# Performance work log

Measured on AMD Instinct MI355X. Metric: run time of the kernel, lower is better.

Reference implementation:

```python
import jax, jax.numpy as jnp
import numpy as np

SIGMA = 5.0  # matches init_kwargs sigma


def so3_exp_map(w):
    """Rodrigues formula. w: [..., 3] axis-angle -> [..., 3, 3] rotation."""
    theta = jnp.sqrt(jnp.sum(w * w, axis=-1) + 1e-12)            # [...]
    wx, wy, wz = w[..., 0], w[..., 1], w[..., 2]
    z = jnp.zeros_like(wx)
    # normalized skew matrix K = hat(w) / theta
    K = jnp.stack([z, -wz, wy,
                   wz, z, -wx,
                   -wy, wx, z], axis=-1).reshape(w.shape[:-1] + (3, 3))
    K = K / theta[..., None, None]
    s = jnp.sin(theta)[..., None, None]
    c = (1.0 - jnp.cos(theta))[..., None, None]
    I = jnp.eye(3, dtype=w.dtype)
    return I + s * K + c * (K @ K)


def setup_inputs() -> dict:
    key = jax.random.key(0)
    k1, k2, k3, k4, k5 = jax.random.split(key, 5)
    P, N, E = 65536, 512, 4096
    # spread points/control points over a volume where sigma=5 is a meaningful scale
    points = jax.random.normal(k1, (P, 3), dtype=jnp.float32) * 10.0
    control_points = jax.random.normal(k2, (N, 3), dtype=jnp.float32) * 10.0
    rot_vec = jax.random.normal(k3, (N, 3), dtype=jnp.float32) * 0.1
    t = jax.random.normal(k4, (N, 3), dtype=jnp.float32) * 0.1
    edges = jax.random.randint(k5, (E, 2), 0, N, dtype=jnp.int64)
    return {"points": points, "control_points": control_points,
            "rot_vec": rot_vec, "t": t, "edges": edges}


def reference(points, control_points, rot_vec, t, edges):
    # ---- warp_points ----
    # local: [P, N, 3]
    local = points[:, None, :] - control_points[None, :, :]
    skin = jnp.exp(-jnp.sum(local * local, axis=-1) / (2.0 * SIGMA * SIGMA))  # [P, N]
    skin = skin / (jnp.sum(skin, axis=-1, keepdims=True) + 1e-5)
    R = so3_exp_map(rot_vec)                                    # [N, 3, 3]
    warped = (jnp.einsum('nij,pnj->pni', R, local)
              + t[None, :, :] + control_points[None, :, :])     # [P, N, 3]
    warped = jnp.sum(warped * skin[..., None], axis=1)          # [P, 3]
    # ---- reg_term ----
    i, j = edges[:, 0], edges[:, 1]
    ci, cj = control_points[i], control_points[j]               # [E, 3]
    ti, tj = t[i], t[j]
    Ri = R[i]                                                   # [E, 3, 3]
    resid = jnp.einsum('mij,mj->mi', Ri, cj - ci) + ci + ti - (cj + tj)
    reg = jnp.sum(resid * resid)
    return warped, reg
```

## Files before the change

kernel.cpp:

```cpp
#include <hip/hip_runtime.h>
#include <math.h>


constexpr int NP = 65536;
constexpr int NN = 512;
constexpr int NE = 4096;
constexpr int PPB = 256;
constexpr int CH = 4;
constexpr int NPC = NN / CH;
constexpr float KEXP = -0.02f * 1.44269504088896340736f;
constexpr float M2K = -2.0f * KEXP;

#if defined(__has_builtin)
#if __has_builtin(__builtin_amdgcn_exp2f)
#define FAST_EXP2(x) __builtin_amdgcn_exp2f(x)
#endif
#endif
#ifndef FAST_EXP2
#define FAST_EXP2(x) exp2f(x)
#endif

__device__ __forceinline__ void rodrigues(float wx, float wy, float wz, float* R) {
    float t2 = wx * wx + wy * wy + wz * wz + 1e-12f;
    float th = sqrtf(t2);
    float inv = 1.0f / th;
    float kx = wx * inv, ky = wy * inv, kz = wz * inv;
    float s = sinf(th);
    float c = 1.0f - cosf(th);
    float kxky = kx * ky, kxkz = kx * kz, kykz = ky * kz;
    R[0] = 1.0f - c * (ky * ky + kz * kz);
    R[1] = -s * kz + c * kxky;
    R[2] =  s * ky + c * kxkz;
    R[3] =  s * kz + c * kxky;
    R[4] = 1.0f - c * (kx * kx + kz * kz);
    R[5] = -s * kx + c * kykz;
    R[6] = -s * ky + c * kxkz;
    R[7] =  s * kx + c * kykz;
    R[8] = 1.0f - c * (kx * kx + ky * ky);
}

__global__ __launch_bounds__(1024) void deform_kernel(
    const float* __restrict__ points,
    const float* __restrict__ cps,
    const float* __restrict__ rot,
    const float* __restrict__ tr,
    const int* __restrict__ edges,
    float* __restrict__ out)
{
    __shared__ float nd[NN * 16];
    __shared__ float4 red[CH - 1][PPB];
    __shared__ float red2[16];

    const int bid = blockIdx.x;
    const int tid = threadIdx.x;

    if (bid < NP / PPB) {
        for (int n = tid; n < NN; n += 1024) {
            float R[9];
            rodrigues(rot[3 * n + 0], rot[3 * n + 1], rot[3 * n + 2], R);
            float cx = cps[3 * n + 0], cy = cps[3 * n + 1], cz = cps[3 * n + 2];
            float tx = tr[3 * n + 0], ty = tr[3 * n + 1], tz = tr[3 * n + 2];
            float bx = tx + cx - (R[0] * cx + R[1] * cy + R[2] * cz);
            float by = ty + cy - (R[3] * cx + R[4] * cy + R[5] * cz);
            float bz = tz + cz - (R[6] * cx + R[7] * cy + R[8] * cz);
            float kc2 = KEXP * (cx * cx + cy * cy + cz * cz);
            float* r = &nd[n * 16];
            r[0] = R[0]; r[1] = R[1]; r[2] = R[2]; r[3] = R[3];
            r[4] = R[4]; r[5] = R[5]; r[6] = R[6]; r[7] = R[7];
            r[8] = R[8]; r[9] = bx;  r[10] = by;  r[11] = bz;
            r[12] = cx;  r[13] = cy; r[14] = cz;  r[15] = kc2;
        }
        __syncthreads();

        const int pt = tid & (PPB - 1);
        const int chunk = tid >> 8;
        const int p = bid * PPB + pt;
        const float px = points[3 * p + 0];
        const float py = points[3 * p + 1];
        const float pz = points[3 * p + 2];
        const float kp2 = KEXP * (px * px + py * py + pz * pz);

        float ax = 0.0f, ay = 0.0f, az = 0.0f, wsum = 0.0f;
        const float* base = &nd[chunk * NPC * 16];

        #pragma unroll 4
        for (int n = 0; n < NPC; ++n) {
            const float4* q = (const float4*)(base + n * 16);
            float4 q0 = q[0];
            float4 q1 = q[1];
            float4 q2 = q[2];
            float4 q3 = q[3];
            float dot = fmaf(q3.x, px, fmaf(q3.y, py, q3.z * pz));
            float w = FAST_EXP2(fmaf(M2K, dot, kp2 + q3.w));
            float yx = fmaf(q0.x, px, fmaf(q0.y, py, fmaf(q0.z, pz, q2.y)));
            float yy = fmaf(q0.w, px, fmaf(q1.x, py, fmaf(q1.y, pz, q2.z)));
            float yz = fmaf(q1.z, px, fmaf(q1.w, py, fmaf(q2.x, pz, q2.w)));
            wsum += w;
            ax = fmaf(w, yx, ax);
            ay = fmaf(w, yy, ay);
            az = fmaf(w, yz, az);
        }

        if (chunk != 0) {
            red[chunk - 1][pt] = make_float4(ax, ay, az, wsum);
        }
        __syncthreads();
        if (chunk == 0) {
            #pragma unroll
            for (int r = 0; r < CH - 1; ++r) {
                float4 v = red[r][pt];
                ax += v.x; ay += v.y; az += v.z; wsum += v.w;
            }
            float invw = 1.0f / (wsum + 1e-5f);
            out[3 * p + 0] = ax * invw;
            out[3 * p + 1] = ay * invw;
            out[3 * p + 2] = az * invw;
        }
    } else {
        float acc = 0.0f;
        for (int e = tid; e < NE; e += 1024) {
            int i = edges[2 * e + 0];
            int j = edges[2 * e + 1];
            float R[9];
            rodrigues(rot[3 * i + 0], rot[3 * i + 1], rot[3 * i + 2], R);
            float cix = cps[3 * i + 0], ciy = cps[3 * i + 1], ciz = cps[3 * i + 2];
            float cjx = cps[3 * j + 0], cjy = cps[3 * j + 1], cjz = cps[3 * j + 2];
            float dx = cjx - cix, dy = cjy - ciy, dz = cjz - ciz;
            float rx = fmaf(R[0], dx, fmaf(R[1], dy, R[2] * dz)) + cix + tr[3 * i + 0] - cjx - tr[3 * j + 0];
            float ry = fmaf(R[3], dx, fmaf(R[4], dy, R[5] * dz)) + ciy + tr[3 * i + 1] - cjy - tr[3 * j + 1];
            float rz = fmaf(R[6], dx, fmaf(R[7], dy, R[8] * dz)) + ciz + tr[3 * i + 2] - cjz - tr[3 * j + 2];
            acc += rx * rx + ry * ry + rz * rz;
        }
        #pragma unroll
        for (int off = 32; off > 0; off >>= 1)
            acc += __shfl_down(acc, off, 64);
        int wid = tid >> 6;
        if ((tid & 63) == 0) red2[wid] = acc;
        __syncthreads();
        if (tid == 0) {
            float s = 0.0f;
            #pragma unroll
            for (int i = 0; i < 16; ++i) s += red2[i];
            out[3 * NP] = s;
        }
    }
}

extern "C" void kernel_launch(void* const* d_in, const int* in_sizes, int n_in,
                              void* d_out, int out_size, void* d_ws, size_t ws_size,
                              hipStream_t stream) {
    const float* points = (const float*)d_in[0];
    const float* cps    = (const float*)d_in[1];
    const float* rot    = (const float*)d_in[2];
    const float* tr     = (const float*)d_in[3];
    const int*   edges  = (const int*)d_in[4];
    float* out = (float*)d_out;
    deform_kernel<<<NP / PPB + 1, 1024, 0, stream>>>(points, cps, rot, tr, edges, out);
}
```

Measured before the change: 89.34 us.

## Register-block four points per thread and split control points into sixteen chunks

Each thread now handles four points, so every control-point record read from LDS is reused across four points instead of one. Control points are split into sixteen chunks per 64-thread wavefront group, and partial sums are combined with a tree reduction through shared memory. Points are loaded and outputs stored as float4 vectors. The cost targeted is LDS bandwidth per FLOP. In exchange it adds register pressure, more reduction barriers, and a larger shared reduction buffer.

```diff
diff --git a/kernel.cpp b/kernel.cpp
--- a/kernel.cpp
+++ b/kernel.cpp
@@ -5,8 +5,10 @@
 constexpr int NP = 65536;
 constexpr int NN = 512;
 constexpr int NE = 4096;
-constexpr int PPB = 256;
-constexpr int CH = 4;
+constexpr int PPT = 4;
+constexpr int CH = 16;
+constexpr int TPC = 64;
+constexpr int PPB = TPC * PPT;
 constexpr int NPC = NN / CH;
 constexpr float KEXP = -0.02f * 1.44269504088896340736f;
 constexpr float M2K = -2.0f * KEXP;
@@ -48,14 +50,15 @@
     float* __restrict__ out)
 {
     __shared__ float nd[NN * 16];
-    __shared__ float4 red[CH - 1][PPB];
+    __shared__ float4 red[CH / 2][PPB];
     __shared__ float red2[16];
 
     const int bid = blockIdx.x;
     const int tid = threadIdx.x;
 
     if (bid < NP / PPB) {
-        for (int n = tid; n < NN; n += 1024) {
+        if (tid < NN) {
+            int n = tid;
             float R[9];
             rodrigues(rot[3 * n + 0], rot[3 * n + 1], rot[3 * n + 2], R);
             float cx = cps[3 * n + 0], cy = cps[3 * n + 1], cz = cps[3 * n + 2];
@@ -72,49 +75,75 @@
         }
         __syncthreads();
 
-        const int pt = tid & (PPB - 1);
-        const int chunk = tid >> 8;
-        const int p = bid * PPB + pt;
-        const float px = points[3 * p + 0];
-        const float py = points[3 * p + 1];
-        const float pz = points[3 * p + 2];
-        const float kp2 = KEXP * (px * px + py * py + pz * pz);
+        const int chunk = tid >> 6;
+        const int tslot = tid & 63;
+        const int p0 = bid * PPB + tslot * PPT;
 
-        float ax = 0.0f, ay = 0.0f, az = 0.0f, wsum = 0.0f;
+        const float4* pv = (const float4*)(points + 3 * p0);
+        float4 va = pv[0], vb = pv[1], vc = pv[2];
+        float px[PPT] = {va.x, va.w, vb.z, vc.y};
+        float py[PPT] = {va.y, vb.x, vb.w, vc.z};
+        float pz[PPT] = {va.z, vb.y, vc.x, vc.w};
+        float kp2[PPT];
+        #pragma unroll
+        for (int k = 0; k < PPT; ++k)
+            kp2[k] = KEXP * (px[k] * px[k] + py[k] * py[k] + pz[k] * pz[k]);
+
+        float ax[PPT] = {0,0,0,0}, ay[PPT] = {0,0,0,0}, az[PPT] = {0,0,0,0}, ws[PPT] = {0,0,0,0};
         const float* base = &nd[chunk * NPC * 16];
 
-        #pragma unroll 4
+        #pragma unroll 2
         for (int n = 0; n < NPC; ++n) {
             const float4* q = (const float4*)(base + n * 16);
             float4 q0 = q[0];
             float4 q1 = q[1];
             float4 q2 = q[2];
             float4 q3 = q[3];
-            float dot = fmaf(q3.x, px, fmaf(q3.y, py, q3.z * pz));
-            float w = FAST_EXP2(fmaf(M2K, dot, kp2 + q3.w));
-            float yx = fmaf(q0.x, px, fmaf(q0.y, py, fmaf(q0.z, pz, q2.y)));
-            float yy = fmaf(q0.w, px, fmaf(q1.x, py, fmaf(q1.y, pz, q2.z)));
-            float yz = fmaf(q1.z, px, fmaf(q1.w, py, fmaf(q2.x, pz, q2.w)));
-            wsum += w;
-            ax = fmaf(w, yx, ax);
-            ay = fmaf(w, yy, ay);
-            az = fmaf(w, yz, az);
+            #pragma unroll
+            for (int k = 0; k < PPT; ++k) {
+                float dot = fmaf(q3.x, px[k], fmaf(q3.y, py[k], q3.z * pz[k]));
+                float w = FAST_EXP2(fmaf(M2K, dot, kp2[k] + q3.w));
+                float yx = fmaf(q0.x, px[k], fmaf(q0.y, py[k], fmaf(q0.z, pz[k], q2.y)));
+                float yy = fmaf(q0.w, px[k], fmaf(q1.x, py[k], fmaf(q1.y, pz[k], q2.z)));
+                float yz = fmaf(q1.z, px[k], fmaf(q1.w, py[k], fmaf(q2.x, pz[k], q2.w)));
+                ws[k] += w;
+                ax[k] = fmaf(w, yx, ax[k]);
+                ay[k] = fmaf(w, yy, ay[k]);
+                az[k] = fmaf(w, yz, az[k]);
+            }
         }
 
-        if (chunk != 0) {
-            red[chunk - 1][pt] = make_float4(ax, ay, az, wsum);
+        #pragma unroll
+        for (int s = CH / 2; s >= 1; s >>= 1) {
+            if (chunk >= s && chunk < 2 * s) {
+                #pragma unroll
+                for (int k = 0; k < PPT; ++k)
+                    red[chunk - s][tslot * PPT + k] = make_float4(ax[k], ay[k], az[k], ws[k]);
+            }
+            __syncthreads();
+            if (chunk < s) {
+                #pragma unroll
+                for (int k = 0; k < PPT; ++k) {
+                    float4 v = red[chunk][tslot * PPT + k];
+                    ax[k] += v.x; ay[k] += v.y; az[k] += v.z; ws[k] += v.w;
+                }
+            }
+            __syncthreads();
         }
-        __syncthreads();
+
         if (chunk == 0) {
+            float o[12];
             #pragma unroll
-            for (int r = 0; r < CH - 1; ++r) {
-                float4 v = red[r][pt];
-                ax += v.x; ay += v.y; az += v.z; wsum += v.w;
+            for (int k = 0; k < PPT; ++k) {
+                float invw = 1.0f / (ws[k] + 1e-5f);
+                o[3 * k + 0] = ax[k] * invw;
+                o[3 * k + 1] = ay[k] * invw;
+                o[3 * k + 2] = az[k] * invw;
             }
-            float invw = 1.0f / (wsum + 1e-5f);
-            out[3 * p + 0] = ax * invw;
-            out[3 * p + 1] = ay * invw;
-            out[3 * p + 2] = az * invw;
+            float4* ov = (float4*)(out + 3 * p0);
+            ov[0] = make_float4(o[0], o[1], o[2], o[3]);
+            ov[1] = make_float4(o[4], o[5], o[6], o[7]);
+            ov[2] = make_float4(o[8], o[9], o[10], o[11]);
         }
     } else {
         float acc = 0.0f;
```

Result: faster. 85.94 us (-3.8%).

## Split prep into separate kernel and stream node table via scalar loads

Applied to the files above, without the earlier changes.

Moves per-node Rodrigues and bias precomputation into a small prep kernel that writes a 16-float table to workspace, instead of recomputing it into shared memory in every block. The main warp kernel then reads each node record with inline-asm s_load_dwordx16 into scalar registers, so the LDS reads and the per-block prep and barrier go away. Blocks now handle 128 points with 8 node chunks per point. Each table read waits immediately on lgkmcnt(0), which serialises scalar-load latency. The extra kernel launch adds a dependency between the two kernels.

```diff
diff --git a/kernel.cpp b/kernel.cpp
--- a/kernel.cpp
+++ b/kernel.cpp
@@ -5,11 +5,13 @@
 constexpr int NP = 65536;
 constexpr int NN = 512;
 constexpr int NE = 4096;
-constexpr int PPB = 256;
-constexpr int CH = 4;
+constexpr int CH = 8;
+constexpr int TPC = 128;
 constexpr int NPC = NN / CH;
 constexpr float KEXP = -0.02f * 1.44269504088896340736f;
 constexpr float M2K = -2.0f * KEXP;
+
+typedef float f16v __attribute__((ext_vector_type(16)));
 
 #if defined(__has_builtin)
 #if __has_builtin(__builtin_amdgcn_exp2f)
@@ -39,23 +41,13 @@
     R[8] = 1.0f - c * (kx * kx + ky * ky);
 }
 
-__global__ __launch_bounds__(1024) void deform_kernel(
-    const float* __restrict__ points,
-    const float* __restrict__ cps,
-    const float* __restrict__ rot,
-    const float* __restrict__ tr,
-    const int* __restrict__ edges,
-    float* __restrict__ out)
-{
-    __shared__ float nd[NN * 16];
-    __shared__ float4 red[CH - 1][PPB];
-    __shared__ float red2[16];
-
-    const int bid = blockIdx.x;
+__global__ void prep_kernel(const float* __restrict__ cps, const float* __restrict__ rot,
+                            const float* __restrict__ tr, const int* __restrict__ edges,
+                            float* __restrict__ tbl, float* __restrict__ out) {
     const int tid = threadIdx.x;
-
-    if (bid < NP / PPB) {
-        for (int n = tid; n < NN; n += 1024) {
+    if (blockIdx.x == 0) {
+        if (tid < NN) {
+            const int n = tid;
             float R[9];
             rodrigues(rot[3 * n + 0], rot[3 * n + 1], rot[3 * n + 2], R);
             float cx = cps[3 * n + 0], cy = cps[3 * n + 1], cz = cps[3 * n + 2];
@@ -64,61 +56,15 @@
             float by = ty + cy - (R[3] * cx + R[4] * cy + R[5] * cz);
             float bz = tz + cz - (R[6] * cx + R[7] * cy + R[8] * cz);
             float kc2 = KEXP * (cx * cx + cy * cy + cz * cz);
-            float* r = &nd[n * 16];
-            r[0] = R[0]; r[1] = R[1]; r[2] = R[2]; r[3] = R[3];
-            r[4] = R[4]; r[5] = R[5]; r[6] = R[6]; r[7] = R[7];
-            r[8] = R[8]; r[9] = bx;  r[10] = by;  r[11] = bz;
-            r[12] = cx;  r[13] = cy; r[14] = cz;  r[15] = kc2;
-        }
-        __syncthreads();
-
-        const int pt = tid & (PPB - 1);
-        const int chunk = tid >> 8;
-        const int p = bid * PPB + pt;
-        const float px = points[3 * p + 0];
-        const float py = points[3 * p + 1];
-        const float pz = points[3 * p + 2];
-        const float kp2 = KEXP * (px * px + py * py + pz * pz);
-
-        float ax = 0.0f, ay = 0.0f, az = 0.0f, wsum = 0.0f;
-        const float* base = &nd[chunk * NPC * 16];
-
-        #pragma unroll 4
-        for (int n = 0; n < NPC; ++n) {
-            const float4* q = (const float4*)(base + n * 16);
-            float4 q0 = q[0];
-            float4 q1 = q[1];
-            float4 q2 = q[2];
-            float4 q3 = q[3];
-            float dot = fmaf(q3.x, px, fmaf(q3.y, py, q3.z * pz));
-            float w = FAST_EXP2(fmaf(M2K, dot, kp2 + q3.w));
-            float yx = fmaf(q0.x, px, fmaf(q0.y, py, fmaf(q0.z, pz, q2.y)));
-            float yy = fmaf(q0.w, px, fmaf(q1.x, py, fmaf(q1.y, pz, q2.z)));
-            float yz = fmaf(q1.z, px, fmaf(q1.w, py, fmaf(q2.x, pz, q2.w)));
-            wsum += w;
-            ax = fmaf(w, yx, ax);
-            ay = fmaf(w, yy, ay);
-            az = fmaf(w, yz, az);
-        }
-
-        if (chunk != 0) {
-            red[chunk - 1][pt] = make_float4(ax, ay, az, wsum);
-        }
-        __syncthreads();
-        if (chunk == 0) {
-            #pragma unroll
-            for (int r = 0; r < CH - 1; ++r) {
-                float4 v = red[r][pt];
-                ax += v.x; ay += v.y; az += v.z; wsum += v.w;
-            }
-            float invw = 1.0f / (wsum + 1e-5f);
-            out[3 * p + 0] = ax * invw;
-            out[3 * p + 1] = ay * invw;
-            out[3 * p + 2] = az * invw;
+            float4* r = (float4*)(tbl + n * 16);
+            r[0] = make_float4(R[0], R[1], R[2], R[3]);
+            r[1] = make_float4(R[4], R[5], R[6], R[7]);
+            r[2] = make_float4(R[8], bx, by, bz);
+            r[3] = make_float4(cx, cy, cz, kc2);
         }
     } else {
         float acc = 0.0f;
-        for (int e = tid; e < NE; e += 1024) {
+        for (int e = tid; e < NE; e += 512) {
             int i = edges[2 * e + 0];
             int j = edges[2 * e + 1];
             float R[9];
@@ -131,6 +77,7 @@
             float rz = fmaf(R[6], dx, fmaf(R[7], dy, R[8] * dz)) + ciz + tr[3 * i + 2] - cjz - tr[3 * j + 2];
             acc += rx * rx + ry * ry + rz * rz;
         }
+        __shared__ float red2[8];
         #pragma unroll
         for (int off = 32; off > 0; off >>= 1)
             acc += __shfl_down(acc, off, 64);
@@ -140,9 +87,62 @@
         if (tid == 0) {
             float s = 0.0f;
             #pragma unroll
-            for (int i = 0; i < 16; ++i) s += red2[i];
+            for (int i = 0; i < 8; ++i) s += red2[i];
             out[3 * NP] = s;
         }
+    }
+}
+
+__global__ __launch_bounds__(1024, 8) void warp_kernel(
+    const float* __restrict__ points,
+    const float* __restrict__ tbl,
+    float* __restrict__ out)
+{
+    __shared__ float4 red[CH - 1][TPC];
+
+    const int tid = threadIdx.x;
+    const int pt = tid & (TPC - 1);
+    const int chunk = tid >> 7;
+    const int p = blockIdx.x * TPC + pt;
+
+    const float px = points[3 * p + 0];
+    const float py = points[3 * p + 1];
+    const float pz = points[3 * p + 2];
+    const float kp2 = KEXP * (px * px + py * py + pz * pz);
+
+    float ax = 0.0f, ay = 0.0f, az = 0.0f, ws = 0.0f;
+
+    const float* ap = tbl + (size_t)(unsigned)__builtin_amdgcn_readfirstlane(chunk * (NPC * 16));
+
+    for (int n = 0; n < NPC; ++n) {
+        f16v r;
+        asm("s_load_dwordx16 %0, %1, 0x0\n\ts_waitcnt lgkmcnt(0)"
+            : "=s"(r) : "s"(ap));
+        ap += 16;
+        float dot = fmaf(r[12], px, fmaf(r[13], py, r[14] * pz));
+        float arg = fmaf(M2K, dot, kp2 + r[15]);
+        float w = FAST_EXP2(arg);
+        float yx = fmaf(r[0], px, fmaf(r[1], py, fmaf(r[2], pz, r[9])));
+        float yy = fmaf(r[3], px, fmaf(r[4], py, fmaf(r[5], pz, r[10])));
+        float yz = fmaf(r[6], px, fmaf(r[7], py, fmaf(r[8], pz, r[11])));
+        ws += w;
+        ax = fmaf(w, yx, ax);
+        ay = fmaf(w, yy, ay);
+        az = fmaf(w, yz, az);
+    }
+
+    if (chunk != 0) red[chunk - 1][pt] = make_float4(ax, ay, az, ws);
+    __syncthreads();
+    if (chunk == 0) {
+        #pragma unroll
+        for (int s = 0; s < CH - 1; ++s) {
+            float4 v = red[s][pt];
+            ax += v.x; ay += v.y; az += v.z; ws += v.w;
+        }
+        float invw = 1.0f / (ws + 1e-5f);
+        out[3 * p + 0] = ax * invw;
+        out[3 * p + 1] = ay * invw;
+        out[3 * p + 2] = az * invw;
     }
 }
 
@@ -155,5 +155,8 @@
     const float* tr     = (const float*)d_in[3];
     const int*   edges  = (const int*)d_in[4];
     float* out = (float*)d_out;
-    deform_kernel<<<NP / PPB + 1, 1024, 0, stream>>>(points, cps, rot, tr, edges, out);
+    float* tbl = (float*)d_ws;
+
+    prep_kernel<<<2, 512, 0, stream>>>(cps, rot, tr, edges, tbl, out);
+    warp_kernel<<<NP / TPC, 1024, 0, stream>>>(points, tbl, out);
 }
```

Measured after the change: 92.39 us. 1.03x slower.

## Register-tile eight points per thread with packed FP32 math and fused reg term

Applied to the files above, without the earlier changes.

Each thread now processes 8 points as packed float2 vectors, so every control-point record loaded from LDS is reused across 8 points, and the math can map to packed FMA instructions. The 512 control points are split across 32 chunks. Partial sums are reduced with a cross-half-wave shuffle and then a tree reduction through LDS. The separate regularisation block is removed: each block handles 16 edges using the precomputed shared table and atomically adds into the scalar output. Risks: the atomicAdd relies on the output already being zero, higher register pressure, and extra synchronisation in the tree reduction.

```diff
diff --git a/kernel.cpp b/kernel.cpp
--- a/kernel.cpp
+++ b/kernel.cpp
@@ -6,10 +6,13 @@
 constexpr int NN = 512;
 constexpr int NE = 4096;
 constexpr int PPB = 256;
-constexpr int CH = 4;
+constexpr int PPT = 8;
+constexpr int CH = 32;
 constexpr int NPC = NN / CH;
 constexpr float KEXP = -0.02f * 1.44269504088896340736f;
 constexpr float M2K = -2.0f * KEXP;
+
+typedef float f2 __attribute__((ext_vector_type(2)));
 
 #if defined(__has_builtin)
 #if __has_builtin(__builtin_amdgcn_exp2f)
@@ -19,6 +22,14 @@
 #ifndef FAST_EXP2
 #define FAST_EXP2(x) exp2f(x)
 #endif
+
+__device__ __forceinline__ f2 b2(float s) { f2 r; r.x = s; r.y = s; return r; }
+__device__ __forceinline__ f2 fm(f2 a, f2 b, f2 c) { return __builtin_elementwise_fma(a, b, c); }
+__device__ __forceinline__ f2 xadd32(f2 v) {
+    v.x += __shfl_xor(v.x, 32, 64);
+    v.y += __shfl_xor(v.y, 32, 64);
+    return v;
+}
 
 __device__ __forceinline__ void rodrigues(float wx, float wy, float wz, float* R) {
     float t2 = wx * wx + wy * wy + wz * wz + 1e-12f;
@@ -39,7 +50,7 @@
     R[8] = 1.0f - c * (kx * kx + ky * ky);
 }
 
-__global__ __launch_bounds__(1024) void deform_kernel(
+__global__ __launch_bounds__(1024, 4) void deform_kernel(
     const float* __restrict__ points,
     const float* __restrict__ cps,
     const float* __restrict__ rot,
@@ -48,101 +59,135 @@
     float* __restrict__ out)
 {
     __shared__ float nd[NN * 16];
-    __shared__ float4 red[CH - 1][PPB];
-    __shared__ float red2[16];
+    __shared__ float4 stab[NN];
+    __shared__ float4 slab[8][PPB];
 
     const int bid = blockIdx.x;
     const int tid = threadIdx.x;
 
-    if (bid < NP / PPB) {
-        for (int n = tid; n < NN; n += 1024) {
-            float R[9];
-            rodrigues(rot[3 * n + 0], rot[3 * n + 1], rot[3 * n + 2], R);
-            float cx = cps[3 * n + 0], cy = cps[3 * n + 1], cz = cps[3 * n + 2];
-            float tx = tr[3 * n + 0], ty = tr[3 * n + 1], tz = tr[3 * n + 2];
-            float bx = tx + cx - (R[0] * cx + R[1] * cy + R[2] * cz);
-            float by = ty + cy - (R[3] * cx + R[4] * cy + R[5] * cz);
-            float bz = tz + cz - (R[6] * cx + R[7] * cy + R[8] * cz);
-            float kc2 = KEXP * (cx * cx + cy * cy + cz * cz);
-            float* r = &nd[n * 16];
-            r[0] = R[0]; r[1] = R[1]; r[2] = R[2]; r[3] = R[3];
-            r[4] = R[4]; r[5] = R[5]; r[6] = R[6]; r[7] = R[7];
-            r[8] = R[8]; r[9] = bx;  r[10] = by;  r[11] = bz;
-            r[12] = cx;  r[13] = cy; r[14] = cz;  r[15] = kc2;
+    if (tid < NN) {
+        const int n = tid;
+        float R[9];
+        rodrigues(rot[3 * n + 0], rot[3 * n + 1], rot[3 * n + 2], R);
+        float cx = cps[3 * n + 0], cy = cps[3 * n + 1], cz = cps[3 * n + 2];
+        float tx = tr[3 * n + 0], ty = tr[3 * n + 1], tz = tr[3 * n + 2];
+        float bx = tx + cx - (R[0] * cx + R[1] * cy + R[2] * cz);
+        float by = ty + cy - (R[3] * cx + R[4] * cy + R[5] * cz);
+        float bz = tz + cz - (R[6] * cx + R[7] * cy + R[8] * cz);
+        float kc2 = KEXP * (cx * cx + cy * cy + cz * cz);
+        float4* r = (float4*)(&nd[n * 16]);
+        r[0] = make_float4(R[0], R[1], R[2], R[3]);
+        r[1] = make_float4(R[4], R[5], R[6], R[7]);
+        r[2] = make_float4(R[8], bx, by, bz);
+        r[3] = make_float4(cx, cy, cz, kc2);
+        stab[n] = make_float4(cx + tx, cy + ty, cz + tz, 0.0f);
+    }
+    __syncthreads();
+
+    if (tid < 16) {
+        const int e = bid * 16 + tid;
+        const int i = edges[2 * e + 0];
+        const int j = edges[2 * e + 1];
+        const float4* ri = (const float4*)(&nd[i * 16]);
+        float4 q0 = ri[0], q1 = ri[1], q2 = ri[2];
+        float4 cj = ((const float4*)(&nd[j * 16]))[3];
+        float4 sj = stab[j];
+        float rx = fmaf(q0.x, cj.x, fmaf(q0.y, cj.y, fmaf(q0.z, cj.z, q2.y))) - sj.x;
+        float ry = fmaf(q0.w, cj.x, fmaf(q1.x, cj.y, fmaf(q1.y, cj.z, q2.z))) - sj.y;
+        float rz = fmaf(q1.z, cj.x, fmaf(q1.w, cj.y, fmaf(q2.x, cj.z, q2.w))) - sj.z;
+        float acc = rx * rx + ry * ry + rz * rz;
+        #pragma unroll
+        for (int off = 8; off > 0; off >>= 1)
+            acc += __shfl_down(acc, off, 16);
+        if (tid == 0) atomicAdd(out + 3 * NP, acc);
+    }
+
+    const int pslot = tid & 31;
+    const int chunk = tid >> 5;
+    const int p0 = bid * PPB + pslot * PPT;
+
+    const float4* pv = (const float4*)(points + 3 * p0);
+    float4 A = pv[0], B = pv[1], Cv = pv[2], D = pv[3], E = pv[4], F = pv[5];
+    f2 px[4], py[4], pz[4];
+    px[0].x=A.x;  px[0].y=A.w;  py[0].x=A.y;  py[0].y=B.x;  pz[0].x=A.z;  pz[0].y=B.y;
+    px[1].x=B.z;  px[1].y=Cv.y; py[1].x=B.w;  py[1].y=Cv.z; pz[1].x=Cv.x; pz[1].y=Cv.w;
+    px[2].x=D.x;  px[2].y=D.w;  py[2].x=D.y;  py[2].y=E.x;  pz[2].x=D.z;  pz[2].y=E.y;
+    px[3].x=E.z;  px[3].y=F.y;  py[3].x=E.w;  py[3].y=F.z;  pz[3].x=F.x;  pz[3].y=F.w;
+
+    f2 kp2[4], ax[4], ay[4], az[4], ws[4];
+    #pragma unroll
+    for (int k = 0; k < 4; ++k) {
+        kp2[k] = b2(KEXP) * (px[k] * px[k] + py[k] * py[k] + pz[k] * pz[k]);
+        ax[k] = b2(0.0f); ay[k] = b2(0.0f); az[k] = b2(0.0f); ws[k] = b2(0.0f);
+    }
+
+    const float* base = &nd[chunk * NPC * 16];
+    #pragma unroll 2
+    for (int n = 0; n < NPC; ++n) {
+        const float4* q = (const float4*)(base + n * 16);
+        float4 q0 = q[0], q1 = q[1], q2 = q[2], q3 = q[3];
+        #pragma unroll
+        for (int k = 0; k < 4; ++k) {
+            f2 dot = fm(b2(q3.x), px[k], fm(b2(q3.y), py[k], b2(q3.z) * pz[k]));
+            f2 arg = fm(b2(M2K), dot, kp2[k] + b2(q3.w));
+            f2 w; w.x = FAST_EXP2(arg.x); w.y = FAST_EXP2(arg.y);
+            f2 yx = fm(b2(q0.x), px[k], fm(b2(q0.y), py[k], fm(b2(q0.z), pz[k], b2(q2.y))));
+            f2 yy = fm(b2(q0.w), px[k], fm(b2(q1.x), py[k], fm(b2(q1.y), pz[k], b2(q2.z))));
+            f2 yz = fm(b2(q1.z), px[k], fm(b2(q1.w), py[k], fm(b2(q2.x), pz[k], b2(q2.w))));
+            ws[k] += w;
+            ax[k] = fm(w, yx, ax[k]);
+            ay[k] = fm(w, yy, ay[k]);
+            az[k] = fm(w, yz, az[k]);
+        }
+    }
+
+    #pragma unroll
+    for (int k = 0; k < 4; ++k) {
+        ax[k] = xadd32(ax[k]); ay[k] = xadd32(ay[k]);
+        az[k] = xadd32(az[k]); ws[k] = xadd32(ws[k]);
+    }
+
+    const int wv = tid >> 6;
+    const bool lo = (tid & 32) == 0;
+    #pragma unroll
+    for (int s = 8; s >= 1; s >>= 1) {
+        if (lo && wv >= s && wv < 2 * s) {
+            #pragma unroll
+            for (int k = 0; k < 4; ++k) {
+                int i0 = pslot * 8 + ((2 * k + pslot) & 7);
+                int i1 = pslot * 8 + ((2 * k + 1 + pslot) & 7);
+                slab[wv - s][i0] = make_float4(ax[k].x, ay[k].x, az[k].x, ws[k].x);
+                slab[wv - s][i1] = make_float4(ax[k].y, ay[k].y, az[k].y, ws[k].y);
+            }
         }
         __syncthreads();
-
-        const int pt = tid & (PPB - 1);
-        const int chunk = tid >> 8;
-        const int p = bid * PPB + pt;
-        const float px = points[3 * p + 0];
-        const float py = points[3 * p + 1];
-        const float pz = points[3 * p + 2];
-        const float kp2 = KEXP * (px * px + py * py + pz * pz);
-
-        float ax = 0.0f, ay = 0.0f, az = 0.0f, wsum = 0.0f;
-        const float* base = &nd[chunk * NPC * 16];
-
-        #pragma unroll 4
-        for (int n = 0; n < NPC; ++n) {
-            const float4* q = (const float4*)(base + n * 16);
-            float4 q0 = q[0];
-            float4 q1 = q[1];
-            float4 q2 = q[2];
-            float4 q3 = q[3];
-            float dot = fmaf(q3.x, px, fmaf(q3.y, py, q3.z * pz));
-            float w = FAST_EXP2(fmaf(M2K, dot, kp2 + q3.w));
-            float yx = fmaf(q0.x, px, fmaf(q0.y, py, fmaf(q0.z, pz, q2.y)));
-            float yy = fmaf(q0.w, px, fmaf(q1.x, py, fmaf(q1.y, pz, q2.z)));
-            float yz = fmaf(q1.z, px, fmaf(q1.w, py, fmaf(q2.x, pz, q2.w)));
-            wsum += w;
-            ax = fmaf(w, yx, ax);
-            ay = fmaf(w, yy, ay);
-            az = fmaf(w, yz, az);
-        }
-
-        if (chunk != 0) {
-            red[chunk - 1][pt] = make_float4(ax, ay, az, wsum);
+        if (lo && wv < s) {
+            #pragma unroll
+            for (int k = 0; k < 4; ++k) {
+                int i0 = pslot * 8 + ((2 * k + pslot) & 7);
+                int i1 = pslot * 8 + ((2 * k + 1 + pslot) & 7);
+                float4 v0 = slab[wv][i0];
+                float4 v1 = slab[wv][i1];
+                ax[k].x += v0.x; ay[k].x += v0.y; az[k].x += v0.z; ws[k].x += v0.w;
+                ax[k].y += v1.x; ay[k].y += v1.y; az[k].y += v1.z; ws[k].y += v1.w;
+            }
         }
         __syncthreads();
-        if (chunk == 0) {
-            #pragma unroll
-            for (int r = 0; r < CH - 1; ++r) {
-                float4 v = red[r][pt];
-                ax += v.x; ay += v.y; az += v.z; wsum += v.w;
-            }
-            float invw = 1.0f / (wsum + 1e-5f);
-            out[3 * p + 0] = ax * invw;
-            out[3 * p + 1] = ay * invw;
-            out[3 * p + 2] = az * invw;
-        }
-    } else {
-        float acc = 0.0f;
-        for (int e = tid; e < NE; e += 1024) {
-            int i = edges[2 * e + 0];
-            int j = edges[2 * e + 1];
-            float R[9];
-            rodrigues(rot[3 * i + 0], rot[3 * i + 1], rot[3 * i + 2], R);
-            float cix = cps[3 * i + 0], ciy = cps[3 * i + 1], ciz = cps[3 * i + 2];
-            float cjx = cps[3 * j + 0], cjy = cps[3 * j + 1], cjz = cps[3 * j + 2];
-            float dx = cjx - cix, dy = cjy - ciy, dz = cjz - ciz;
-            float rx = fmaf(R[0], dx, fmaf(R[1], dy, R[2] * dz)) + cix + tr[3 * i + 0] - cjx - tr[3 * j + 0];
-            float ry = fmaf(R[3], dx, fmaf(R[4], dy, R[5] * dz)) + ciy + tr[3 * i + 1] - cjy - tr[3 * j + 1];
-            float rz = fmaf(R[6], dx, fmaf(R[7], dy, R[8] * dz)) + ciz + tr[3 * i + 2] - cjz - tr[3 * j + 2];
-            acc += rx * rx + ry * ry + rz * rz;
-        }
-        #pragma unroll
-        for (int off = 32; off > 0; off >>= 1)
-            acc += __shfl_down(acc, off, 64);
-        int wid = tid >> 6;
-        if ((tid & 63) == 0) red2[wid] = acc;
-        __syncthreads();
-        if (tid == 0) {
-            float s = 0.0f;
-            #pragma unroll
-            for (int i = 0; i < 16; ++i) s += red2[i];
-            out[3 * NP] = s;
-        }
+    }
+
+    if (tid < 32) {
+        float o[24];
+        #pragma unroll
+        for (int k = 0; k < 4; ++k) {
+            float ivx = 1.0f / (ws[k].x + 1e-5f);
+            float ivy = 1.0f / (ws[k].y + 1e-5f);
+            o[6 * k + 0] = ax[k].x * ivx; o[6 * k + 1] = ay[k].x * ivx; o[6 * k + 2] = az[k].x * ivx;
+            o[6 * k + 3] = ax[k].y * ivy; o[6 * k + 4] = ay[k].y * ivy; o[6 * k + 5] = az[k].y * ivy;
+        }
+        float4* ov = (float4*)(out + 3 * p0);
+        #pragma unroll
+        for (int q = 0; q < 6; ++q)
+            ov[q] = make_float4(o[4 * q], o[4 * q + 1], o[4 * q + 2], o[4 * q + 3]);
     }
 }
 
@@ -155,5 +200,5 @@
     const float* tr     = (const float*)d_in[3];
     const int*   edges  = (const int*)d_in[4];
     float* out = (float*)d_out;
-    deform_kernel<<<NP / PPB + 1, 1024, 0, stream>>>(points, cps, rot, tr, edges, out);
-}
+    deform_kernel<<<NP / PPB, 1024, 0, stream>>>(points, cps, rot, tr, edges, out);
+}
```

New measurement: 80.16 us. -10.3%, faster.
